# Kernel optimization log

Hardware: AMD Instinct MI355X
Metric: run time of the kernel (lower is better)

## Reference

```python
import jax, jax.numpy as jnp
import numpy as np

ORDER = 5
NB_DF = 96
LOOKAHEAD = 0


def setup_inputs() -> dict:
    key = jax.random.key(0)
    k1, k2 = jax.random.split(key)
    B, T, F = 32, 2000, 481
    spec = jax.random.normal(k1, (B, 1, T, F, 2), dtype=jnp.float32)
    coefs = jax.random.normal(k2, (B, ORDER, T, NB_DF, 2), dtype=jnp.float32)
    return {"spec": spec, "coefs": coefs}


def reference(spec, coefs):
    # spec: [B,1,T,F,2], coefs: [B,order,T,nb_df,2]
    B, C, T, F, _ = spec.shape
    # real/imag of the deep-filtered frequency band only ([B,1,T,nb_df])
    sr = spec[..., :NB_DF, 0]
    si = spec[..., :NB_DF, 1]
    pad_before = ORDER - 1 - LOOKAHEAD
    pad_cfg = ((0, 0), (0, 0), (pad_before, LOOKAHEAD), (0, 0))
    sr_p = jnp.pad(sr, pad_cfg)
    si_p = jnp.pad(si, pad_cfg)
    # unfold over time: lag n window = padded[:, :, n:n+T]  -> [order,B,1,T,nb_df]
    sur = jnp.stack([sr_p[:, :, n:n + T] for n in range(ORDER)], axis=0)
    sui = jnp.stack([si_p[:, :, n:n + T] for n in range(ORDER)], axis=0)
    # coefs viewed as [B,1,order,T,nb_df] -> align as [order,B,1,T,nb_df]
    cr = jnp.transpose(coefs[..., 0], (1, 0, 2, 3))[:, :, None]
    ci = jnp.transpose(coefs[..., 1], (1, 0, 2, 3))[:, :, None]
    # complex contraction over the order (time-lag) axis
    out_r = jnp.sum(sur * cr - sui * ci, axis=0)  # [B,1,T,nb_df]
    out_i = jnp.sum(sur * ci + sui * cr, axis=0)
    spec_f = jnp.stack([out_r, out_i], axis=-1)   # [B,1,T,nb_df,2]
    # write filtered band back into the full spectrogram
    return spec.at[..., :NB_DF, :].set(spec_f)
```

## Files before the change

### kernel.cpp

```cpp
#include <hip/hip_runtime.h>


constexpr int ORDER = 5;
constexpr int NB_DF = 96;
constexpr int T_DIM = 2000;
constexpr int F_DIM = 481;
constexpr int B_DIM = 32;

constexpr int F4    = NB_DF / 2;
constexpr int BLOCK = 256;

constexpr int FIR_THREADS = B_DIM * T_DIM * F4;
constexpr int FIR_BLOCKS  = FIR_THREADS / BLOCK;

constexpr int COPY_BLOCKS = FIR_BLOCKS;
constexpr int COPY_F      = F_DIM - NB_DF;
constexpr int N_ROWS      = B_DIM * T_DIM;
constexpr unsigned COPY_ELEMS  = (unsigned)N_ROWS * (unsigned)COPY_F;
constexpr unsigned COPY_STRIDE = (unsigned)COPY_BLOCKS * BLOCK;

__global__ __launch_bounds__(BLOCK, 6) void ApplyDF_29231547416739_kernel(
    const float2* __restrict__ spec,
    const float4* __restrict__ coefs4,
    float2* __restrict__ out)
{
    const int bid = blockIdx.x;
    const int tid = threadIdx.x;
    const int half = bid >> 1;

    if ((bid & 1) == 0) {
        const int flat = half * BLOCK + tid;
        const int col  = flat % F4;
        const int rest = flat / F4;
        const int b    = rest / T_DIM;
        const int t    = rest - b * T_DIM;

        float2 slo[ORDER], shi[ORDER];
#pragma unroll
        for (int n = 0; n < ORDER; ++n) {
            const int tt  = t + n - (ORDER - 1);
            const int ttc = tt >= 0 ? tt : 0;
            const float2* p = spec + ((size_t)b * T_DIM + ttc) * F_DIM + 2 * col;
            float2 lo = p[0];
            float2 hi = p[1];
            if (tt < 0) { lo = make_float2(0.f, 0.f); hi = make_float2(0.f, 0.f); }
            slo[n] = lo; shi[n] = hi;
        }
        float4 c[ORDER];
#pragma unroll
        for (int n = 0; n < ORDER; ++n)
            c[n] = coefs4[(((size_t)b * ORDER + n) * T_DIM + t) * F4 + col];

        float4 acc = make_float4(0.f, 0.f, 0.f, 0.f);
#pragma unroll
        for (int n = 0; n < ORDER; ++n) {
            acc.x = fmaf(slo[n].x, c[n].x, fmaf(-slo[n].y, c[n].y, acc.x));
            acc.y = fmaf(slo[n].x, c[n].y, fmaf( slo[n].y, c[n].x, acc.y));
            acc.z = fmaf(shi[n].x, c[n].z, fmaf(-shi[n].y, c[n].w, acc.z));
            acc.w = fmaf(shi[n].x, c[n].w, fmaf( shi[n].y, c[n].z, acc.w));
        }

        float2* op = out + ((size_t)b * T_DIM + t) * F_DIM + 2 * col;
        op[0] = make_float2(acc.x, acc.y);
        op[1] = make_float2(acc.z, acc.w);
    } else {
        const unsigned base = (unsigned)half * BLOCK + tid;
#pragma unroll
        for (int rep = 0; rep < 2; ++rep) {
            const unsigned i0 = base + (unsigned)(rep * 4) * COPY_STRIDE;
            size_t off[4];
            float2 v[4];
#pragma unroll
            for (int u = 0; u < 4; ++u) {
                const unsigned idx = i0 + (unsigned)u * COPY_STRIDE;
                const unsigned row = idx / COPY_F;
                const unsigned ff  = idx - row * COPY_F + NB_DF;
                off[u] = (size_t)row * F_DIM + ff;
                v[u]   = spec[off[u]];
            }
#pragma unroll
            for (int u = 0; u < 4; ++u) out[off[u]] = v[u];
        }
        if (base < 64000u) {
            const unsigned idx = base + 8u * COPY_STRIDE;
            const unsigned row = idx / COPY_F;
            const unsigned ff  = idx - row * COPY_F + NB_DF;
            const size_t off   = (size_t)row * F_DIM + ff;
            out[off] = spec[off];
        }
    }
}

extern "C" void kernel_launch(void* const* d_in, const int* in_sizes, int n_in,
                              void* d_out, int out_size, void* d_ws, size_t ws_size,
                              hipStream_t stream) {
    const float2* spec   = (const float2*)d_in[0];
    const float4* coefs4 = (const float4*)d_in[1];
    float2* out = (float2*)d_out;

    dim3 grid(FIR_BLOCKS + COPY_BLOCKS);
    dim3 block(BLOCK);
    ApplyDF_29231547416739_kernel<<<grid, block, 0, stream>>>(spec, coefs4, out);
}
```

Measured before the change: 551.7 us.

## Split into full-spectrogram float4 copy kernel followed by FIR-only kernel

Replaces the interleaved FIR/copy blocks of one fused kernel with two launches. The first is a grid-stride float4 copy of the whole spectrogram, and the second is a FIR kernel that overwrites the deep-filter band. The FIR kernel also gets a fast path without clamping for t>=4. The aim is to swap the scattered float2 copy, with its per-element division, for wide coalesced copies. The cost is copying the first 96 bins that get overwritten anyway (about 20% extra copy traffic) plus a second launch that is ordered after the first.

Result: slower. 590.3 us (+7.0%).

```diff
diff --git a/kernel.cpp b/kernel.cpp
--- a/kernel.cpp
+++ b/kernel.cpp
@@ -7,35 +7,60 @@
 constexpr int F_DIM = 481;
 constexpr int B_DIM = 32;
 
-constexpr int F4    = NB_DF / 2;
 constexpr int BLOCK = 256;
 
+constexpr unsigned TOT_FLOATS = (unsigned)B_DIM * T_DIM * F_DIM * 2u;
+constexpr unsigned TOT4       = TOT_FLOATS / 4u;
+constexpr int      COPY_GRID  = 2048;
+constexpr unsigned CS         = (unsigned)COPY_GRID * BLOCK;
+constexpr unsigned FULL_ITERS = TOT4 / (4u * CS);
+constexpr unsigned FULL_END   = FULL_ITERS * 4u * CS;
+
+__global__ __launch_bounds__(BLOCK) void ApplyDF_copy4_kernel(
+    const float4* __restrict__ in, float4* __restrict__ out)
+{
+    const unsigned gid = blockIdx.x * BLOCK + threadIdx.x;
+    for (unsigned j = 0; j < FULL_ITERS; ++j) {
+        const unsigned i0 = gid + j * 4u * CS;
+        float4 v0 = in[i0];
+        float4 v1 = in[i0 + CS];
+        float4 v2 = in[i0 + 2u * CS];
+        float4 v3 = in[i0 + 3u * CS];
+        out[i0]           = v0;
+        out[i0 + CS]      = v1;
+        out[i0 + 2u * CS] = v2;
+        out[i0 + 3u * CS] = v3;
+    }
+    for (unsigned i = FULL_END + gid; i < TOT4; i += CS) out[i] = in[i];
+}
+
+constexpr int F4          = NB_DF / 2;
 constexpr int FIR_THREADS = B_DIM * T_DIM * F4;
 constexpr int FIR_BLOCKS  = FIR_THREADS / BLOCK;
 
-constexpr int COPY_BLOCKS = FIR_BLOCKS;
-constexpr int COPY_F      = F_DIM - NB_DF;
-constexpr int N_ROWS      = B_DIM * T_DIM;
-constexpr unsigned COPY_ELEMS  = (unsigned)N_ROWS * (unsigned)COPY_F;
-constexpr unsigned COPY_STRIDE = (unsigned)COPY_BLOCKS * BLOCK;
-
-__global__ __launch_bounds__(BLOCK, 6) void ApplyDF_29231547416739_kernel(
+__global__ __launch_bounds__(BLOCK, 4) void ApplyDF_29231547416739_kernel(
     const float2* __restrict__ spec,
     const float4* __restrict__ coefs4,
     float2* __restrict__ out)
 {
-    const int bid = blockIdx.x;
-    const int tid = threadIdx.x;
-    const int half = bid >> 1;
+    const int flat = blockIdx.x * BLOCK + threadIdx.x;
+    const int col  = flat % F4;
+    const int rest = flat / F4;
+    const int b    = rest / T_DIM;
+    const int t    = rest - b * T_DIM;
 
-    if ((bid & 1) == 0) {
-        const int flat = half * BLOCK + tid;
-        const int col  = flat % F4;
-        const int rest = flat / F4;
-        const int b    = rest / T_DIM;
-        const int t    = rest - b * T_DIM;
+    const size_t rowbase = (size_t)b * T_DIM + t;
 
-        float2 slo[ORDER], shi[ORDER];
+    float2 slo[ORDER], shi[ORDER];
+    if (t >= ORDER - 1) {
+        const float2* p0 = spec + (rowbase - (ORDER - 1)) * F_DIM + 2 * col;
+#pragma unroll
+        for (int n = 0; n < ORDER; ++n) {
+            const float2* p = p0 + (size_t)n * F_DIM;
+            slo[n] = p[0];
+            shi[n] = p[1];
+        }
+    } else {
 #pragma unroll
         for (int n = 0; n < ORDER; ++n) {
             const int tt  = t + n - (ORDER - 1);
@@ -46,49 +71,25 @@
             if (tt < 0) { lo = make_float2(0.f, 0.f); hi = make_float2(0.f, 0.f); }
             slo[n] = lo; shi[n] = hi;
         }
-        float4 c[ORDER];
+    }
+
+    float4 c[ORDER];
 #pragma unroll
-        for (int n = 0; n < ORDER; ++n)
-            c[n] = coefs4[(((size_t)b * ORDER + n) * T_DIM + t) * F4 + col];
+    for (int n = 0; n < ORDER; ++n)
+        c[n] = coefs4[(((size_t)b * ORDER + n) * T_DIM + t) * F4 + col];
 
-        float4 acc = make_float4(0.f, 0.f, 0.f, 0.f);
+    float4 acc = make_float4(0.f, 0.f, 0.f, 0.f);
 #pragma unroll
-        for (int n = 0; n < ORDER; ++n) {
-            acc.x = fmaf(slo[n].x, c[n].x, fmaf(-slo[n].y, c[n].y, acc.x));
-            acc.y = fmaf(slo[n].x, c[n].y, fmaf( slo[n].y, c[n].x, acc.y));
-            acc.z = fmaf(shi[n].x, c[n].z, fmaf(-shi[n].y, c[n].w, acc.z));
-            acc.w = fmaf(shi[n].x, c[n].w, fmaf( shi[n].y, c[n].z, acc.w));
-        }
+    for (int n = 0; n < ORDER; ++n) {
+        acc.x = fmaf(slo[n].x, c[n].x, fmaf(-slo[n].y, c[n].y, acc.x));
+        acc.y = fmaf(slo[n].x, c[n].y, fmaf( slo[n].y, c[n].x, acc.y));
+        acc.z = fmaf(shi[n].x, c[n].z, fmaf(-shi[n].y, c[n].w, acc.z));
+        acc.w = fmaf(shi[n].x, c[n].w, fmaf( shi[n].y, c[n].z, acc.w));
+    }
 
-        float2* op = out + ((size_t)b * T_DIM + t) * F_DIM + 2 * col;
-        op[0] = make_float2(acc.x, acc.y);
-        op[1] = make_float2(acc.z, acc.w);
-    } else {
-        const unsigned base = (unsigned)half * BLOCK + tid;
-#pragma unroll
-        for (int rep = 0; rep < 2; ++rep) {
-            const unsigned i0 = base + (unsigned)(rep * 4) * COPY_STRIDE;
-            size_t off[4];
-            float2 v[4];
-#pragma unroll
-            for (int u = 0; u < 4; ++u) {
-                const unsigned idx = i0 + (unsigned)u * COPY_STRIDE;
-                const unsigned row = idx / COPY_F;
-                const unsigned ff  = idx - row * COPY_F + NB_DF;
-                off[u] = (size_t)row * F_DIM + ff;
-                v[u]   = spec[off[u]];
-            }
-#pragma unroll
-            for (int u = 0; u < 4; ++u) out[off[u]] = v[u];
-        }
-        if (base < 64000u) {
-            const unsigned idx = base + 8u * COPY_STRIDE;
-            const unsigned row = idx / COPY_F;
-            const unsigned ff  = idx - row * COPY_F + NB_DF;
-            const size_t off   = (size_t)row * F_DIM + ff;
-            out[off] = spec[off];
-        }
-    }
+    float2* op = out + rowbase * F_DIM + 2 * col;
+    op[0] = make_float2(acc.x, acc.y);
+    op[1] = make_float2(acc.z, acc.w);
 }
 
 extern "C" void kernel_launch(void* const* d_in, const int* in_sizes, int n_in,
@@ -98,7 +99,8 @@
     const float4* coefs4 = (const float4*)d_in[1];
     float2* out = (float2*)d_out;
 
-    dim3 grid(FIR_BLOCKS + COPY_BLOCKS);
-    dim3 block(BLOCK);
-    ApplyDF_29231547416739_kernel<<<grid, block, 0, stream>>>(spec, coefs4, out);
+    ApplyDF_copy4_kernel<<<dim3(COPY_GRID), dim3(BLOCK), 0, stream>>>(
+        (const float4*)spec, (float4*)out);
+    ApplyDF_29231547416739_kernel<<<dim3(FIR_BLOCKS), dim3(BLOCK), 0, stream>>>(
+        spec, coefs4, out);
 }
```
